# Optimization experiments

Hardware: AMD Instinct MI355X
Metric: run time of the kernel (lower is better)

## Reference

```python
import jax, jax.numpy as jnp
import numpy as np

B, S, D = 4, 4096, 256
H, K = 4, 64  # num_heads, key_dim
EPS = 1e-3    # Keras LayerNormalization default epsilon
NEG = -1e9    # Keras additive mask constant for float32


def setup_inputs() -> dict:
    key = jax.random.key(0)
    ks = jax.random.split(key, 12)
    sd = 1.0 / np.sqrt(D)
    return {
        "query": jax.random.normal(ks[0], (B, S, D), dtype=jnp.float32),
        "value": jax.random.normal(ks[1], (B, S, D), dtype=jnp.float32),
        "Wq": jax.random.normal(ks[2], (D, H, K), dtype=jnp.float32) * sd,
        "bq": jnp.zeros((H, K), dtype=jnp.float32),
        "Wk": jax.random.normal(ks[3], (D, H, K), dtype=jnp.float32) * sd,
        "bk": jnp.zeros((H, K), dtype=jnp.float32),
        "Wv": jax.random.normal(ks[4], (D, H, K), dtype=jnp.float32) * sd,
        "bv": jnp.zeros((H, K), dtype=jnp.float32),
        "Wo": jax.random.normal(ks[5], (H, K, D), dtype=jnp.float32) * sd,
        "bo": jnp.zeros((D,), dtype=jnp.float32),
        "gamma": jnp.ones((D,), dtype=jnp.float32),
        "beta": jnp.zeros((D,), dtype=jnp.float32),
    }


def reference(query, value, Wq, bq, Wk, bk, Wv, bv, Wo, bo, gamma, beta):
    # Keras MHA(query, value): key defaults to value
    q = jnp.einsum("bsd,dhk->bshk", query, Wq) + bq
    k = jnp.einsum("bsd,dhk->bshk", value, Wk) + bk
    v = jnp.einsum("bsd,dhk->bshk", value, Wv) + bv
    scores = jnp.einsum("bqhk,bshk->bhqs", q, k) / jnp.sqrt(jnp.float32(K))
    # lower-triangular causal mask, applied additively (Keras semantics)
    causal = jnp.tril(jnp.ones((q.shape[1], q.shape[1]), dtype=bool))
    scores = scores + jnp.where(causal, 0.0, NEG)
    attn = jax.nn.softmax(scores, axis=-1)  # [B,H,S,S]
    ctx = jnp.einsum("bhqs,bshk->bqhk", attn, v)
    mha_out = jnp.einsum("bqhk,hkd->bqd", ctx, Wo) + bo
    # residual + LayerNorm (over last axis)
    x = mha_out + query
    mu = jnp.mean(x, axis=-1, keepdims=True)
    var = jnp.mean(jnp.square(x - mu), axis=-1, keepdims=True)
    return (x - mu) * jax.lax.rsqrt(var + EPS) * gamma + beta
```

## Files before the change

### kernel.cpp

```cpp
#include <hip/hip_runtime.h>
#include <hip/hip_bf16.h>
#include <stdint.h>

#define SS 4096
#define DD 256
#define HH 4
#define KK 64
#define ALPHA 0.18033688011112042f

typedef float f32x4 __attribute__((ext_vector_type(4)));
typedef short s16x8 __attribute__((ext_vector_type(8)));
typedef unsigned int u32;

__device__ __forceinline__ unsigned short f2bf(float x) {
  union { float f; unsigned u; } v; v.f = x;
  unsigned r = v.u + 0x7fffu + ((v.u >> 16) & 1u);
  return (unsigned short)(r >> 16);
}

__device__ __forceinline__ u32 cvtpk(float lo, float hi) {
  u32 r;
  asm("v_cvt_pk_bf16_f32 %0, %1, %2" : "=v"(r) : "v"(lo), "v"(hi));
  return r;
}

#define fexp2(x) __builtin_amdgcn_exp2f(x)

__device__ __forceinline__ void gl_lds16(const unsigned short* g, unsigned short* l) {
  __builtin_amdgcn_global_load_lds(
      (const __attribute__((address_space(1))) u32*)g,
      (__attribute__((address_space(3))) u32*)l, 16, 0, 0);
}

__device__ __forceinline__ void acc8(const unsigned short* p, f32x4& a0, f32x4& a1) {
  s16x8 v = *(const s16x8*)p;
  union { u32 u; float f; } c;
  #pragma unroll
  for (int j = 0; j < 4; ++j) { c.u = ((u32)(unsigned short)v[j]) << 16; a0[j] += c.f; }
  #pragma unroll
  for (int j = 0; j < 4; ++j) { c.u = ((u32)(unsigned short)v[4 + j]) << 16; a1[j] += c.f; }
}

__global__ void wprep(const float* __restrict__ Wq, const float* __restrict__ Wk,
                      const float* __restrict__ Wv, const float* __restrict__ Wo,
                      unsigned short* __restrict__ Wt, unsigned short* __restrict__ Wot)
{
  const int blk = blockIdx.x, t = threadIdx.x;
  const int rsub = t >> 4;
  const int c0 = (t & 15) * 16;
  if (blk < 48) {
    const int n = blk * 16 + rsub;
    const float* W = (n < 256) ? Wq : ((n < 512) ? Wk : Wv);
    const int nn = n & 255;
    const float sc = (n < 256) ? ALPHA : 1.0f;
    for (int c = c0; c < c0 + 16; ++c)
      Wt[(size_t)n * 256 + c] = f2bf(sc * W[(size_t)c * 256 + nn]);
  } else {
    const int d = (blk - 48) * 16 + rsub;
    for (int c = c0; c < c0 + 16; ++c)
      Wot[(size_t)d * 256 + c] = f2bf(Wo[(size_t)c * 256 + d]);
  }
}

__global__ __launch_bounds__(256, 3) void qkv_mfma(
    const float* __restrict__ query, const float* __restrict__ value,
    const unsigned short* __restrict__ Wt,
    const float* __restrict__ bq, const float* __restrict__ bk,
    const float* __restrict__ bv,
    unsigned short* __restrict__ qb, unsigned short* __restrict__ kbs,
    unsigned short* __restrict__ vts)
{
  __shared__ __align__(16) unsigned short Xs[64 * 256];

  const int t = threadIdx.x;
  const int w = t >> 6, l = t & 63, lr = l & 15, grp = l >> 4;
  const int mat = (int)(blockIdx.x % 3u);
  const int rb  = (int)(blockIdx.x / 3u);
  const long r0 = (long)rb * 64;

  const float* X = (mat == 0) ? query : value;

  {
    const int row = t >> 2;
    const int c0s = (t & 3) * 64;
    const float* xp = X + (r0 + row) * 256 + c0s;
    const int sw = (row & 7) << 3;
    #pragma unroll
    for (int g = 0; g < 8; ++g) {
      f32x4 x0 = *(const f32x4*)(xp + g * 8);
      f32x4 x1 = *(const f32x4*)(xp + g * 8 + 4);
      union { u32 wd[4]; s16x8 v; } bb;
      bb.wd[0] = cvtpk(x0[0], x0[1]);
      bb.wd[1] = cvtpk(x0[2], x0[3]);
      bb.wd[2] = cvtpk(x1[0], x1[1]);
      bb.wd[3] = cvtpk(x1[2], x1[3]);
      *(s16x8*)&Xs[(row * 256 + c0s + g * 8) ^ sw] = bb.v;
    }
  }
  __syncthreads();

  const int n0 = w * 64;
  const int swr = (lr & 7) << 3;

  f32x4 acc[4][4] = {};

  #pragma unroll 2
  for (int k0 = 0; k0 < 256; k0 += 32) {
    s16x8 xf[4];
    #pragma unroll
    for (int mt = 0; mt < 4; ++mt)
      xf[mt] = *(const s16x8*)&Xs[((mt * 16 + lr) * 256 + k0 + grp * 8) ^ swr];
    #pragma unroll
    for (int nt = 0; nt < 4; ++nt) {
      s16x8 af = *(const s16x8*)(Wt + (size_t)(mat * 256 + n0 + nt * 16 + lr) * 256 + k0 + grp * 8);
      if (mat == 2) {
        #pragma unroll
        for (int mt = 0; mt < 4; ++mt)
          acc[mt][nt] = __builtin_amdgcn_mfma_f32_16x16x32_bf16(xf[mt], af, acc[mt][nt], 0, 0, 0);
      } else {
        #pragma unroll
        for (int mt = 0; mt < 4; ++mt)
          acc[mt][nt] = __builtin_amdgcn_mfma_f32_16x16x32_bf16(af, xf[mt], acc[mt][nt], 0, 0, 0);
      }
    }
  }

  const int b  = (int)(r0 >> 12);
  const int s0 = (int)(r0 & 4095);
  const int kt = s0 >> 6;
  const size_t base = (size_t)(b * 4 + w) * (SS * KK) + (size_t)kt * 4096;

  if (mat == 0) {
    #pragma unroll
    for (int nt = 0; nt < 4; ++nt) {
      const int nk = nt * 16 + grp * 4;
      f32x4 bias = *(const f32x4*)&bq[n0 + nk] * ALPHA;
      #pragma unroll
      for (int mt = 0; mt < 4; ++mt) {
        const int s = s0 + mt * 16 + lr;
        f32x4 o = acc[mt][nt] + bias;
        uint2 pk2; pk2.x = cvtpk(o[0], o[1]); pk2.y = cvtpk(o[2], o[3]);
        *(uint2*)&qb[((size_t)(b * 4 + w) * SS + s) * KK + nk] = pk2;
      }
    }
  } else if (mat == 1) {
    #pragma unroll
    for (int nt = 0; nt < 4; ++nt) {
      const int d0 = nt * 16 + grp * 4;
      const int cc = d0 >> 5, grpk = (d0 >> 3) & 3, jlo = d0 & 7;
      f32x4 bias = *(const f32x4*)&bk[n0 + d0];
      #pragma unroll
      for (int mt = 0; mt < 4; ++mt) {
        const int chunk = ((mt * 2 + cc) * 4 + grpk) * 16 + lr;
        f32x4 o = acc[mt][nt] + bias;
        uint2 pk2; pk2.x = cvtpk(o[0], o[1]); pk2.y = cvtpk(o[2], o[3]);
        *(uint2*)&kbs[base + chunk * 8 + jlo] = pk2;
      }
    }
  } else {
    #pragma unroll
    for (int nt = 0; nt < 4; ++nt) {
      const float bvn = bv[n0 + nt * 16 + lr];
      #pragma unroll
      for (int mt = 0; mt < 4; ++mt) {
        const int cb = (nt * 2 + (mt >> 1)) * 64 + grp * 16 + lr;
        f32x4 o = acc[mt][nt] + bvn;
        uint2 pk2; pk2.x = cvtpk(o[0], o[1]); pk2.y = cvtpk(o[2], o[3]);
        *(uint2*)&vts[base + (size_t)cb * 8 + (mt & 1) * 4] = pk2;
      }
    }
  }
}

__global__ __launch_bounds__(256, 4) void attn(
    const unsigned short* __restrict__ qb,
    const unsigned short* __restrict__ kbs,
    const unsigned short* __restrict__ vts,
    unsigned short* __restrict__ ns0, unsigned short* __restrict__ ns1,
    unsigned short* __restrict__ ns2, unsigned short* __restrict__ ns3,
    float* __restrict__ lb0, float* __restrict__ lb1,
    float* __restrict__ lb2, float* __restrict__ lb3)
{
  __shared__ __align__(16) unsigned short Kl[2][4096];
  __shared__ __align__(16) unsigned short Vl[2][4096];

  const int t = threadIdx.x;
  const int w = t >> 6, l = t & 63, lr = l & 15, grp = l >> 4;
  const int qg = w >> 1, kh = w & 1;

  const int i    = blockIdx.x;
  const int bh   = i & 15;
  const int pr   = (i >> 4) & 31;
  const int role = (i >> 9) & 1;
  const int b = bh >> 2, h = bh & 3;

  const unsigned short* kbase = kbs + (size_t)bh * (SS * KK);
  const unsigned short* vbase = vts + (size_t)bh * (SS * KK);
  const unsigned short* qpb   = qb  + (size_t)bh * (SS * KK);

  int sup = (role == 0) ? pr : (63 - pr);
  const int nsteps = 33 - role;

  s16x8 qf[2][2];
  #pragma unroll
  for (int q2 = 0; q2 < 2; ++q2) {
    const unsigned short* qp = qpb + (size_t)(sup * 64 + qg * 32 + q2 * 16 + lr) * KK;
    qf[q2][0] = *(const s16x8*)(qp + grp * 8);
    qf[q2][1] = *(const s16x8*)(qp + 32 + grp * 8);
  }

  s16x8 ones;
  #pragma unroll
  for (int e = 0; e < 8; ++e) ones[e] = (short)0x3F80;
  const f32x4 minit = {-16.f, -16.f, -16.f, -16.f};

  f32x4 cacc[2][4] = {};
  f32x4 lacc[2] = {};

  const int off0 = (w * 64 + l) * 8;
  const int off1 = ((4 + w) * 64 + l) * 8;

  auto ktfor = [&](int s) {
    return (role == 0) ? ((s <= pr) ? s : (s - (pr + 1))) : (32 - pr + s);
  };
  auto stage = [&](int kt, int bi) {
    const unsigned short* ks = kbase + (size_t)kt * 4096;
    const unsigned short* vs = vbase + (size_t)kt * 4096;
    gl_lds16(ks + off0, &Kl[bi][w * 512]);
    gl_lds16(ks + off1, &Kl[bi][(4 + w) * 512]);
    gl_lds16(vs + off0, &Vl[bi][w * 512]);
    gl_lds16(vs + off1, &Vl[bi][(4 + w) * 512]);
  };

  stage(ktfor(0), 0);
  __syncthreads();

  for (int ss = 0; ss < nsteps; ++ss) {
    const int cur = ss & 1;
    if (ss + 1 < nsteps) stage(ktfor(ss + 1), cur ^ 1);

    const int kt = ktfor(ss);
    const unsigned short* Kb = &Kl[cur][0];
    const unsigned short* Vb = &Vl[cur][0];

    s16x8 kf[4];
    #pragma unroll
    for (int j = 0; j < 4; ++j)
      kf[j] = *(const s16x8*)&Kb[(((kh * 4 + j) * 4 + grp) * 16 + lr) * 8];

    f32x4 sc[2][2];
    #pragma unroll
    for (int q2 = 0; q2 < 2; ++q2) {
      #pragma unroll
      for (int tt = 0; tt < 2; ++tt) {
        f32x4 a = __builtin_amdgcn_mfma_f32_16x16x32_bf16(kf[tt * 2 + 0], qf[q2][0], minit, 0, 0, 0);
        a = __builtin_amdgcn_mfma_f32_16x16x32_bf16(kf[tt * 2 + 1], qf[q2][1], a, 0, 0, 0);
        sc[q2][tt] = a;
      }
    }

    if (kt == sup) {
      #pragma unroll
      for (int q2 = 0; q2 < 2; ++q2) {
        const int qloc = qg * 32 + q2 * 16 + lr;
        #pragma unroll
        for (int tt = 0; tt < 2; ++tt)
          #pragma unroll
          for (int e = 0; e < 4; ++e)
            if (((kh * 2 + tt) * 16 + grp * 4 + e) > qloc) sc[q2][tt][e] += -1.0e9f;
      }
    }

    #pragma unroll
    for (int q2 = 0; q2 < 2; ++q2)
      #pragma unroll
      for (int tt = 0; tt < 2; ++tt)
        #pragma unroll
        for (int e = 0; e < 4; ++e)
          sc[q2][tt][e] = fexp2(sc[q2][tt][e]);

    s16x8 pf[2];
    #pragma unroll
    for (int q2 = 0; q2 < 2; ++q2) {
      union { u32 wd[4]; s16x8 v; } pu;
      pu.wd[0] = cvtpk(sc[q2][0][0], sc[q2][0][1]);
      pu.wd[1] = cvtpk(sc[q2][0][2], sc[q2][0][3]);
      pu.wd[2] = cvtpk(sc[q2][1][0], sc[q2][1][1]);
      pu.wd[3] = cvtpk(sc[q2][1][2], sc[q2][1][3]);
      pf[q2] = pu.v;
    }

    #pragma unroll
    for (int m2 = 0; m2 < 4; ++m2) {
      s16x8 vfr = *(const s16x8*)&Vb[((m2 * 2 + kh) * 64 + l) * 8];
      cacc[0][m2] = __builtin_amdgcn_mfma_f32_16x16x32_bf16(vfr, pf[0], cacc[0][m2], 0, 0, 0);
      cacc[1][m2] = __builtin_amdgcn_mfma_f32_16x16x32_bf16(vfr, pf[1], cacc[1][m2], 0, 0, 0);
    }
    lacc[0] = __builtin_amdgcn_mfma_f32_16x16x32_bf16(ones, pf[0], lacc[0], 0, 0, 0);
    lacc[1] = __builtin_amdgcn_mfma_f32_16x16x32_bf16(ones, pf[1], lacc[1], 0, 0, 0);

    if (role == 0 && ss == pr) {
      unsigned short* nsl = kh ? ns1 : ns0;
      float* lbl = kh ? lb1 : lb0;
      #pragma unroll
      for (int q2 = 0; q2 < 2; ++q2) {
        const int rowg = sup * 64 + qg * 32 + q2 * 16 + lr;
        unsigned short* np_ = nsl + ((size_t)((b << 12) + rowg)) * 256 + h * 64;
        #pragma unroll
        for (int m2 = 0; m2 < 4; ++m2) {
          uint2 pk2; pk2.x = cvtpk(cacc[q2][m2][0], cacc[q2][m2][1]);
          pk2.y = cvtpk(cacc[q2][m2][2], cacc[q2][m2][3]);
          *(uint2*)&np_[m2 * 16 + grp * 4] = pk2;
          cacc[q2][m2] = (f32x4){0.f, 0.f, 0.f, 0.f};
        }
        if (grp == 0) lbl[(bh << 12) + rowg] = lacc[q2][0];
        lacc[q2] = (f32x4){0.f, 0.f, 0.f, 0.f};
      }
      sup = 63 - pr;
      #pragma unroll
      for (int q2 = 0; q2 < 2; ++q2) {
        const unsigned short* qp = qpb + (size_t)(sup * 64 + qg * 32 + q2 * 16 + lr) * KK;
        qf[q2][0] = *(const s16x8*)(qp + grp * 8);
        qf[q2][1] = *(const s16x8*)(qp + 32 + grp * 8);
      }
    }
    __syncthreads();
  }

  if (role == 0) {
    unsigned short* nsl = kh ? ns1 : ns0;
    float* lbl = kh ? lb1 : lb0;
    #pragma unroll
    for (int q2 = 0; q2 < 2; ++q2) {
      const int rowg = sup * 64 + qg * 32 + q2 * 16 + lr;
      unsigned short* np_ = nsl + ((size_t)((b << 12) + rowg)) * 256 + h * 64;
      #pragma unroll
      for (int m2 = 0; m2 < 4; ++m2) {
        uint2 pk2; pk2.x = cvtpk(cacc[q2][m2][0], cacc[q2][m2][1]);
        pk2.y = cvtpk(cacc[q2][m2][2], cacc[q2][m2][3]);
        *(uint2*)&np_[m2 * 16 + grp * 4] = pk2;
      }
      if (grp == 0) lbl[(bh << 12) + rowg] = lacc[q2][0];
    }
  } else {
    unsigned short* nsl = kh ? ns3 : ns2;
    float* lbl = kh ? lb3 : lb2;
    #pragma unroll
    for (int q2 = 0; q2 < 2; ++q2) {
      const int rowg = sup * 64 + qg * 32 + q2 * 16 + lr;
      unsigned short* np_ = nsl + ((size_t)((b << 11) + (rowg - 2048))) * 256 + h * 64;
      #pragma unroll
      for (int m2 = 0; m2 < 4; ++m2) {
        uint2 pk2; pk2.x = cvtpk(cacc[q2][m2][0], cacc[q2][m2][1]);
        pk2.y = cvtpk(cacc[q2][m2][2], cacc[q2][m2][3]);
        *(uint2*)&np_[m2 * 16 + grp * 4] = pk2;
      }
      if (grp == 0) lbl[(bh << 11) + (rowg - 2048)] = lacc[q2][0];
    }
  }
}

__global__ __launch_bounds__(256, 4) void oproj_ln(
    const unsigned short* __restrict__ ns0, const unsigned short* __restrict__ ns1,
    const unsigned short* __restrict__ ns2, const unsigned short* __restrict__ ns3,
    const float* __restrict__ lb0, const float* __restrict__ lb1,
    const float* __restrict__ lb2, const float* __restrict__ lb3,
    const unsigned short* __restrict__ Wot,
    const float* __restrict__ bo, const float* __restrict__ query,
    const float* __restrict__ gamma, const float* __restrict__ beta,
    float* __restrict__ out)
{
  __shared__ __align__(16) float redS[32][4];
  __shared__ __align__(16) float redQ[32][4];

  const int t = threadIdx.x;
  const int w = t >> 6, l = t & 63, lr = l & 15, grp = l >> 4;
  const long r0 = (long)blockIdx.x * 32;
  const int n0c = w * 64;
  const int b = (int)(r0 >> 12);
  const bool heavy = ((r0 >> 11) & 1) != 0;

  float invl[2][4];
  #pragma unroll
  for (int mt = 0; mt < 2; ++mt) {
    const int grow = (int)r0 + mt * 16 + lr;
    #pragma unroll
    for (int h = 0; h < 4; ++h) {
      const int i12 = ((b * 4 + h) << 12) + (grow & 4095);
      float lv = lb0[i12] + lb1[i12];
      if (heavy) {
        const int i11 = ((b * 4 + h) << 11) + (grow & 2047);
        lv += lb2[i11] + lb3[i11];
      }
      invl[mt][h] = 1.0f / lv;
    }
  }

  f32x4 acc[2][4] = {};

  #pragma unroll
  for (int k0 = 0; k0 < 256; k0 += 32) {
    s16x8 bfr[2];
    #pragma unroll
    for (int mt = 0; mt < 2; ++mt) {
      const int grow = (int)r0 + mt * 16 + lr;
      const int c = k0 + grp * 8;
      f32x4 a0 = {0.f, 0.f, 0.f, 0.f}, a1 = {0.f, 0.f, 0.f, 0.f};
      const size_t o01 = (size_t)grow * 256 + c;
      acc8(ns0 + o01, a0, a1);
      acc8(ns1 + o01, a0, a1);
      if (heavy) {
        const size_t o23 = ((size_t)((b << 11) + (grow & 2047))) * 256 + c;
        acc8(ns2 + o23, a0, a1);
        acc8(ns3 + o23, a0, a1);
      }
      const float iv = invl[mt][k0 >> 6];
      a0 *= iv; a1 *= iv;
      union { u32 wd[4]; s16x8 v; } bb;
      bb.wd[0] = cvtpk(a0[0], a0[1]);
      bb.wd[1] = cvtpk(a0[2], a0[3]);
      bb.wd[2] = cvtpk(a1[0], a1[1]);
      bb.wd[3] = cvtpk(a1[2], a1[3]);
      bfr[mt] = bb.v;
    }
    #pragma unroll
    for (int nt = 0; nt < 4; ++nt) {
      s16x8 af = *(const s16x8*)(Wot + (size_t)(n0c + nt * 16 + lr) * 256 + k0 + grp * 8);
      acc[0][nt] = __builtin_amdgcn_mfma_f32_16x16x32_bf16(af, bfr[0], acc[0][nt], 0, 0, 0);
      acc[1][nt] = __builtin_amdgcn_mfma_f32_16x16x32_bf16(af, bfr[1], acc[1][nt], 0, 0, 0);
    }
  }

  float sm[2] = {0.f, 0.f}, sq[2] = {0.f, 0.f};
  #pragma unroll
  for (int mt = 0; mt < 2; ++mt) {
    const long s = r0 + mt * 16 + lr;
    #pragma unroll
    for (int nt = 0; nt < 4; ++nt) {
      const int n = n0c + nt * 16 + grp * 4;
      f32x4 v = acc[mt][nt] + *(const f32x4*)&bo[n] + *(const f32x4*)&query[s * 256 + n];
      acc[mt][nt] = v;
      sm[mt] += v[0] + v[1] + v[2] + v[3];
      sq[mt] += v[0]*v[0] + v[1]*v[1] + v[2]*v[2] + v[3]*v[3];
    }
    sm[mt] += __shfl_xor(sm[mt], 16); sm[mt] += __shfl_xor(sm[mt], 32);
    sq[mt] += __shfl_xor(sq[mt], 16); sq[mt] += __shfl_xor(sq[mt], 32);
  }
  if (grp == 0) {
    redS[0 * 16 + lr][w] = sm[0]; redQ[0 * 16 + lr][w] = sq[0];
    redS[1 * 16 + lr][w] = sm[1]; redQ[1 * 16 + lr][w] = sq[1];
  }
  __syncthreads();

  #pragma unroll
  for (int mt = 0; mt < 2; ++mt) {
    f32x4 s4 = *(const f32x4*)&redS[mt * 16 + lr][0];
    f32x4 q4 = *(const f32x4*)&redQ[mt * 16 + lr][0];
    const float tot = s4[0] + s4[1] + s4[2] + s4[3];
    const float tq  = q4[0] + q4[1] + q4[2] + q4[3];
    const float mu  = tot * 0.00390625f;
    const float var = tq * 0.00390625f - mu * mu;
    const float rs  = rsqrtf(var + 1.0e-3f);
    const long s = r0 + mt * 16 + lr;
    #pragma unroll
    for (int nt = 0; nt < 4; ++nt) {
      const int n = n0c + nt * 16 + grp * 4;
      f32x4 g = *(const f32x4*)&gamma[n];
      f32x4 bt = *(const f32x4*)&beta[n];
      f32x4 o = (acc[mt][nt] - mu) * rs * g + bt;
      *(f32x4*)&out[s * 256 + n] = o;
    }
  }
}

extern "C" void kernel_launch(void* const* d_in, const int* in_sizes, int n_in,
                              void* d_out, int out_size, void* d_ws, size_t ws_size,
                              hipStream_t stream) {
  const float* query = (const float*)d_in[0];
  const float* value = (const float*)d_in[1];
  const float* Wq    = (const float*)d_in[2];
  const float* bq    = (const float*)d_in[3];
  const float* Wk    = (const float*)d_in[4];
  const float* bk    = (const float*)d_in[5];
  const float* Wv    = (const float*)d_in[6];
  const float* bv    = (const float*)d_in[7];
  const float* Wo    = (const float*)d_in[8];
  const float* bo    = (const float*)d_in[9];
  const float* gamma = (const float*)d_in[10];
  const float* beta  = (const float*)d_in[11];
  float* out = (float*)d_out;

  char* ws = (char*)d_ws;
  unsigned short* qb  = (unsigned short*)ws;
  unsigned short* kbs = (unsigned short*)(ws + ((size_t)8  << 20));
  unsigned short* vts = (unsigned short*)(ws + ((size_t)16 << 20));
  unsigned short* ns0 = (unsigned short*)(ws + ((size_t)24 << 20));
  unsigned short* ns1 = (unsigned short*)(ws + ((size_t)32 << 20));
  unsigned short* ns2 = (unsigned short*)(ws + ((size_t)40 << 20));
  unsigned short* ns3 = (unsigned short*)(ws + ((size_t)44 << 20));
  float* lb0 = (float*)(ws + ((size_t)48 << 20));
  float* lb1 = (float*)(ws + ((size_t)48 << 20) + ((size_t)256 << 10));
  float* lb2 = (float*)(ws + ((size_t)48 << 20) + ((size_t)512 << 10));
  float* lb3 = (float*)(ws + ((size_t)48 << 20) + ((size_t)640 << 10));
  unsigned short* Wt  = (unsigned short*)(ws + ((size_t)48 << 20) + ((size_t)768 << 10));
  unsigned short* Wot = Wt + (size_t)768 * 256;

  wprep<<<64, 256, 0, stream>>>(Wq, Wk, Wv, Wo, Wt, Wot);
  qkv_mfma<<<768, 256, 0, stream>>>(query, value, Wt, bq, bk, bv, qb, kbs, vts);
  attn<<<1024, 256, 0, stream>>>(qb, kbs, vts, ns0, ns1, ns2, ns3, lb0, lb1, lb2, lb3);
  oproj_ln<<<512, 256, 0, stream>>>(ns0, ns1, ns2, ns3, lb0, lb1, lb2, lb3,
                                    Wot, bo, query, gamma, beta, out);
}
```

Measured before the change: 110.6 us.

## Merge key-half partial attention sums in LDS before writing to global

The attention kernel now reduces the two key-half waves' partial context and row-sum accumulators through shared memory, reusing the K/V staging buffers, before storing. Only one partial buffer per role is written, instead of two. This halves the partial-output traffic that the attention kernel writes and the output-projection kernel reads back. It also adds s_setprio around the MFMA blocks and spreads the weight-prep kernel over more blocks, at the cost of extra barriers and LDS round trips at flush points.

```diff
diff --git a/kernel.cpp b/kernel.cpp
--- a/kernel.cpp
+++ b/kernel.cpp
@@ -46,18 +46,20 @@
                       unsigned short* __restrict__ Wt, unsigned short* __restrict__ Wot)
 {
   const int blk = blockIdx.x, t = threadIdx.x;
-  const int rsub = t >> 4;
-  const int c0 = (t & 15) * 16;
-  if (blk < 48) {
-    const int n = blk * 16 + rsub;
+  const int rsub = t >> 6;
+  const int c0 = (t & 63) * 4;
+  if (blk < 192) {
+    const int n = blk * 4 + rsub;
     const float* W = (n < 256) ? Wq : ((n < 512) ? Wk : Wv);
     const int nn = n & 255;
     const float sc = (n < 256) ? ALPHA : 1.0f;
-    for (int c = c0; c < c0 + 16; ++c)
+    #pragma unroll
+    for (int c = c0; c < c0 + 4; ++c)
       Wt[(size_t)n * 256 + c] = f2bf(sc * W[(size_t)c * 256 + nn]);
   } else {
-    const int d = (blk - 48) * 16 + rsub;
-    for (int c = c0; c < c0 + 16; ++c)
+    const int d = (blk - 192) * 4 + rsub;
+    #pragma unroll
+    for (int c = c0; c < c0 + 4; ++c)
       Wot[(size_t)d * 256 + c] = f2bf(Wo[(size_t)c * 256 + d]);
   }
 }
@@ -176,13 +178,12 @@
     const unsigned short* __restrict__ qb,
     const unsigned short* __restrict__ kbs,
     const unsigned short* __restrict__ vts,
-    unsigned short* __restrict__ ns0, unsigned short* __restrict__ ns1,
-    unsigned short* __restrict__ ns2, unsigned short* __restrict__ ns3,
-    float* __restrict__ lb0, float* __restrict__ lb1,
-    float* __restrict__ lb2, float* __restrict__ lb3)
+    unsigned short* __restrict__ ns0, unsigned short* __restrict__ ns2,
+    float* __restrict__ lb0, float* __restrict__ lb2)
 {
   __shared__ __align__(16) unsigned short Kl[2][4096];
   __shared__ __align__(16) unsigned short Vl[2][4096];
+  __shared__ float lred[2][2][16];
 
   const int t = threadIdx.x;
   const int w = t >> 6, l = t & 63, lr = l & 15, grp = l >> 4;
@@ -232,6 +233,31 @@
     gl_lds16(vs + off1, &Vl[bi][(4 + w) * 512]);
   };
 
+  auto merge_kh = [&](int cur) {
+    float* mb0 = (float*)&Kl[cur][0];
+    float* mb1 = (float*)&Vl[cur][0];
+    if (kh == 1) {
+      #pragma unroll
+      for (int m2 = 0; m2 < 4; ++m2)
+        #pragma unroll
+        for (int e = 0; e < 4; ++e) {
+          mb0[(m2 * 4 + e) * 128 + qg * 64 + l] = cacc[0][m2][e];
+          mb1[(m2 * 4 + e) * 128 + qg * 64 + l] = cacc[1][m2][e];
+        }
+      if (grp == 0) { lred[qg][0][lr] = lacc[0][0]; lred[qg][1][lr] = lacc[1][0]; }
+    }
+    __syncthreads();
+    if (kh == 0) {
+      #pragma unroll
+      for (int m2 = 0; m2 < 4; ++m2)
+        #pragma unroll
+        for (int e = 0; e < 4; ++e) {
+          cacc[0][m2][e] += mb0[(m2 * 4 + e) * 128 + qg * 64 + l];
+          cacc[1][m2][e] += mb1[(m2 * 4 + e) * 128 + qg * 64 + l];
+        }
+    }
+  };
+
   stage(ktfor(0), 0);
   __syncthreads();
 
@@ -248,6 +274,7 @@
     for (int j = 0; j < 4; ++j)
       kf[j] = *(const s16x8*)&Kb[(((kh * 4 + j) * 4 + grp) * 16 + lr) * 8];
 
+    __builtin_amdgcn_s_setprio(1);
     f32x4 sc[2][2];
     #pragma unroll
     for (int q2 = 0; q2 < 2; ++q2) {
@@ -258,6 +285,7 @@
         sc[q2][tt] = a;
       }
     }
+    __builtin_amdgcn_s_setprio(0);
 
     if (kt == sup) {
       #pragma unroll
@@ -290,6 +318,7 @@
       pf[q2] = pu.v;
     }
 
+    __builtin_amdgcn_s_setprio(1);
     #pragma unroll
     for (int m2 = 0; m2 < 4; ++m2) {
       s16x8 vfr = *(const s16x8*)&Vb[((m2 * 2 + kh) * 64 + l) * 8];
@@ -298,73 +327,76 @@
     }
     lacc[0] = __builtin_amdgcn_mfma_f32_16x16x32_bf16(ones, pf[0], lacc[0], 0, 0, 0);
     lacc[1] = __builtin_amdgcn_mfma_f32_16x16x32_bf16(ones, pf[1], lacc[1], 0, 0, 0);
+    __builtin_amdgcn_s_setprio(0);
 
     if (role == 0 && ss == pr) {
-      unsigned short* nsl = kh ? ns1 : ns0;
-      float* lbl = kh ? lb1 : lb0;
+      __syncthreads();
+      merge_kh(cur);
+      if (kh == 0) {
+        #pragma unroll
+        for (int q2 = 0; q2 < 2; ++q2) {
+          const int rowg = sup * 64 + qg * 32 + q2 * 16 + lr;
+          unsigned short* np_ = ns0 + ((size_t)((b << 12) + rowg)) * 256 + h * 64;
+          #pragma unroll
+          for (int m2 = 0; m2 < 4; ++m2) {
+            uint2 pk2; pk2.x = cvtpk(cacc[q2][m2][0], cacc[q2][m2][1]);
+            pk2.y = cvtpk(cacc[q2][m2][2], cacc[q2][m2][3]);
+            *(uint2*)&np_[m2 * 16 + grp * 4] = pk2;
+          }
+          if (grp == 0) lb0[(bh << 12) + rowg] = lacc[q2][0] + lred[qg][q2][lr];
+        }
+      }
+      #pragma unroll
+      for (int q2 = 0; q2 < 2; ++q2) {
+        cacc[q2][0] = cacc[q2][1] = cacc[q2][2] = cacc[q2][3] = (f32x4){0.f, 0.f, 0.f, 0.f};
+        lacc[q2] = (f32x4){0.f, 0.f, 0.f, 0.f};
+      }
+      sup = 63 - pr;
+      #pragma unroll
+      for (int q2 = 0; q2 < 2; ++q2) {
+        const unsigned short* qp = qpb + (size_t)(sup * 64 + qg * 32 + q2 * 16 + lr) * KK;
+        qf[q2][0] = *(const s16x8*)(qp + grp * 8);
+        qf[q2][1] = *(const s16x8*)(qp + 32 + grp * 8);
+      }
+    }
+    __syncthreads();
+  }
+
+  merge_kh((nsteps - 1) & 1);
+  if (kh == 0) {
+    if (role == 0) {
       #pragma unroll
       for (int q2 = 0; q2 < 2; ++q2) {
         const int rowg = sup * 64 + qg * 32 + q2 * 16 + lr;
-        unsigned short* np_ = nsl + ((size_t)((b << 12) + rowg)) * 256 + h * 64;
+        unsigned short* np_ = ns0 + ((size_t)((b << 12) + rowg)) * 256 + h * 64;
         #pragma unroll
         for (int m2 = 0; m2 < 4; ++m2) {
           uint2 pk2; pk2.x = cvtpk(cacc[q2][m2][0], cacc[q2][m2][1]);
           pk2.y = cvtpk(cacc[q2][m2][2], cacc[q2][m2][3]);
           *(uint2*)&np_[m2 * 16 + grp * 4] = pk2;
-          cacc[q2][m2] = (f32x4){0.f, 0.f, 0.f, 0.f};
         }
-        if (grp == 0) lbl[(bh << 12) + rowg] = lacc[q2][0];
-        lacc[q2] = (f32x4){0.f, 0.f, 0.f, 0.f};
-      }
-      sup = 63 - pr;
+        if (grp == 0) lb0[(bh << 12) + rowg] = lacc[q2][0] + lred[qg][q2][lr];
+      }
+    } else {
       #pragma unroll
       for (int q2 = 0; q2 < 2; ++q2) {
-        const unsigned short* qp = qpb + (size_t)(sup * 64 + qg * 32 + q2 * 16 + lr) * KK;
-        qf[q2][0] = *(const s16x8*)(qp + grp * 8);
-        qf[q2][1] = *(const s16x8*)(qp + 32 + grp * 8);
-      }
-    }
-    __syncthreads();
-  }
-
-  if (role == 0) {
-    unsigned short* nsl = kh ? ns1 : ns0;
-    float* lbl = kh ? lb1 : lb0;
-    #pragma unroll
-    for (int q2 = 0; q2 < 2; ++q2) {
-      const int rowg = sup * 64 + qg * 32 + q2 * 16 + lr;
-      unsigned short* np_ = nsl + ((size_t)((b << 12) + rowg)) * 256 + h * 64;
-      #pragma unroll
-      for (int m2 = 0; m2 < 4; ++m2) {
-        uint2 pk2; pk2.x = cvtpk(cacc[q2][m2][0], cacc[q2][m2][1]);
-        pk2.y = cvtpk(cacc[q2][m2][2], cacc[q2][m2][3]);
-        *(uint2*)&np_[m2 * 16 + grp * 4] = pk2;
-      }
-      if (grp == 0) lbl[(bh << 12) + rowg] = lacc[q2][0];
-    }
-  } else {
-    unsigned short* nsl = kh ? ns3 : ns2;
-    float* lbl = kh ? lb3 : lb2;
-    #pragma unroll
-    for (int q2 = 0; q2 < 2; ++q2) {
-      const int rowg = sup * 64 + qg * 32 + q2 * 16 + lr;
-      unsigned short* np_ = nsl + ((size_t)((b << 11) + (rowg - 2048))) * 256 + h * 64;
-      #pragma unroll
-      for (int m2 = 0; m2 < 4; ++m2) {
-        uint2 pk2; pk2.x = cvtpk(cacc[q2][m2][0], cacc[q2][m2][1]);
-        pk2.y = cvtpk(cacc[q2][m2][2], cacc[q2][m2][3]);
-        *(uint2*)&np_[m2 * 16 + grp * 4] = pk2;
-      }
-      if (grp == 0) lbl[(bh << 11) + (rowg - 2048)] = lacc[q2][0];
+        const int rowg = sup * 64 + qg * 32 + q2 * 16 + lr;
+        unsigned short* np_ = ns2 + ((size_t)((b << 11) + (rowg - 2048))) * 256 + h * 64;
+        #pragma unroll
+        for (int m2 = 0; m2 < 4; ++m2) {
+          uint2 pk2; pk2.x = cvtpk(cacc[q2][m2][0], cacc[q2][m2][1]);
+          pk2.y = cvtpk(cacc[q2][m2][2], cacc[q2][m2][3]);
+          *(uint2*)&np_[m2 * 16 + grp * 4] = pk2;
+        }
+        if (grp == 0) lb2[(bh << 11) + (rowg - 2048)] = lacc[q2][0] + lred[qg][q2][lr];
+      }
     }
   }
 }
 
 __global__ __launch_bounds__(256, 4) void oproj_ln(
-    const unsigned short* __restrict__ ns0, const unsigned short* __restrict__ ns1,
-    const unsigned short* __restrict__ ns2, const unsigned short* __restrict__ ns3,
-    const float* __restrict__ lb0, const float* __restrict__ lb1,
-    const float* __restrict__ lb2, const float* __restrict__ lb3,
+    const unsigned short* __restrict__ ns0, const unsigned short* __restrict__ ns2,
+    const float* __restrict__ lb0, const float* __restrict__ lb2,
     const unsigned short* __restrict__ Wot,
     const float* __restrict__ bo, const float* __restrict__ query,
     const float* __restrict__ gamma, const float* __restrict__ beta,
@@ -386,12 +418,8 @@
     const int grow = (int)r0 + mt * 16 + lr;
     #pragma unroll
     for (int h = 0; h < 4; ++h) {
-      const int i12 = ((b * 4 + h) << 12) + (grow & 4095);
-      float lv = lb0[i12] + lb1[i12];
-      if (heavy) {
-        const int i11 = ((b * 4 + h) << 11) + (grow & 2047);
-        lv += lb2[i11] + lb3[i11];
-      }
+      float lv = lb0[((b * 4 + h) << 12) + (grow & 4095)];
+      if (heavy) lv += lb2[((b * 4 + h) << 11) + (grow & 2047)];
       invl[mt][h] = 1.0f / lv;
     }
   }
@@ -406,14 +434,9 @@
       const int grow = (int)r0 + mt * 16 + lr;
       const int c = k0 + grp * 8;
       f32x4 a0 = {0.f, 0.f, 0.f, 0.f}, a1 = {0.f, 0.f, 0.f, 0.f};
-      const size_t o01 = (size_t)grow * 256 + c;
-      acc8(ns0 + o01, a0, a1);
-      acc8(ns1 + o01, a0, a1);
-      if (heavy) {
-        const size_t o23 = ((size_t)((b << 11) + (grow & 2047))) * 256 + c;
-        acc8(ns2 + o23, a0, a1);
-        acc8(ns3 + o23, a0, a1);
-      }
+      acc8(ns0 + (size_t)grow * 256 + c, a0, a1);
+      if (heavy)
+        acc8(ns2 + ((size_t)((b << 11) + (grow & 2047))) * 256 + c, a0, a1);
       const float iv = invl[mt][k0 >> 6];
       a0 *= iv; a1 *= iv;
       union { u32 wd[4]; s16x8 v; } bb;
@@ -495,19 +518,14 @@
   unsigned short* kbs = (unsigned short*)(ws + ((size_t)8  << 20));
   unsigned short* vts = (unsigned short*)(ws + ((size_t)16 << 20));
   unsigned short* ns0 = (unsigned short*)(ws + ((size_t)24 << 20));
-  unsigned short* ns1 = (unsigned short*)(ws + ((size_t)32 << 20));
-  unsigned short* ns2 = (unsigned short*)(ws + ((size_t)40 << 20));
-  unsigned short* ns3 = (unsigned short*)(ws + ((size_t)44 << 20));
-  float* lb0 = (float*)(ws + ((size_t)48 << 20));
-  float* lb1 = (float*)(ws + ((size_t)48 << 20) + ((size_t)256 << 10));
-  float* lb2 = (float*)(ws + ((size_t)48 << 20) + ((size_t)512 << 10));
-  float* lb3 = (float*)(ws + ((size_t)48 << 20) + ((size_t)640 << 10));
-  unsigned short* Wt  = (unsigned short*)(ws + ((size_t)48 << 20) + ((size_t)768 << 10));
+  unsigned short* ns2 = (unsigned short*)(ws + ((size_t)32 << 20));
+  float* lb0 = (float*)(ws + ((size_t)36 << 20));
+  float* lb2 = (float*)(ws + ((size_t)36 << 20) + ((size_t)256 << 10));
+  unsigned short* Wt  = (unsigned short*)(ws + ((size_t)36 << 20) + ((size_t)512 << 10));
   unsigned short* Wot = Wt + (size_t)768 * 256;
 
-  wprep<<<64, 256, 0, stream>>>(Wq, Wk, Wv, Wo, Wt, Wot);
+  wprep<<<256, 256, 0, stream>>>(Wq, Wk, Wv, Wo, Wt, Wot);
   qkv_mfma<<<768, 256, 0, stream>>>(query, value, Wt, bq, bk, bv, qb, kbs, vts);
-  attn<<<1024, 256, 0, stream>>>(qb, kbs, vts, ns0, ns1, ns2, ns3, lb0, lb1, lb2, lb3);
-  oproj_ln<<<512, 256, 0, stream>>>(ns0, ns1, ns2, ns3, lb0, lb1, lb2, lb3,
-                                    Wot, bo, query, gamma, beta, out);
-}
+  attn<<<1024, 256, 0, stream>>>(qb, kbs, vts, ns0, ns2, lb0, lb2);
+  oproj_ln<<<512, 256, 0, stream>>>(ns0, ns2, lb0, lb2, Wot, bo, query, gamma, beta, out);
+}
```

Measured after the change: 101.0 us, median of 2. -8.7%, faster.
